# Kernel tuning notes

Hardware: AMD Instinct MI355X
Metric: run time of the kernel (lower is better)

## Reference

```python
import jax, jax.numpy as jnp
import numpy as np
from jax import lax

DN = ('NHWC', 'HWIO', 'NHWC')
NEG = -1e30  # stand-in for -inf at inactive sites during masked max-pool


def setup_inputs() -> dict:
    key = jax.random.key(0)
    ks = jax.random.split(key, 6)
    B, H, W, Cin = 1024, 21, 21, 200
    x = jax.random.normal(ks[0], (B, H, W, Cin), dtype=jnp.float32)
    mask = jax.random.randint(ks[1], (B, H, W), 0, 2, dtype=jnp.int32)
    W1 = jax.random.normal(ks[2], (2, 2, Cin, 16), dtype=jnp.float32) * 0.05
    W2 = jax.random.normal(ks[3], (5, 5, 16, 32), dtype=jnp.float32) * 0.05
    Wlin = jax.random.normal(ks[4], (32, 2), dtype=jnp.float32) * 0.1
    blin = jax.random.normal(ks[5], (2,), dtype=jnp.float32) * 0.1
    return {"x": x, "mask": mask, "W1": W1, "W2": W2, "Wlin": Wlin, "blin": blin}


def _masked_maxpool(h, m, win, stride):
    # scn.MaxPooling: max over ACTIVE sites in window; output site active iff any input active.
    hm = jnp.where(m > 0, h, NEG)
    out = lax.reduce_window(hm, NEG, lax.max, (1, win, win, 1), (1, stride, stride, 1), 'VALID')
    m_out = lax.reduce_window(m, 0.0, lax.max, (1, win, win, 1), (1, stride, stride, 1), 'VALID')
    return jnp.where(m_out > 0, out, 0.0), m_out


def reference(x, mask, W1, W2, Wlin, blin):
    m = mask.astype(x.dtype)[..., None]          # [B,21,21,1] active-site mask
    h = x * m                                    # inactive sites carry zero features
    # SubmanifoldConvolution(2, 200, 16, filter=2): size-preserving, gathers only
    # active neighbors (zeros elsewhere), outputs only at input active sites.
    h = lax.conv_general_dilated(h, W1, (1, 1), [(0, 1), (0, 1)], dimension_numbers=DN)
    h = h * m                                    # [B,21,21,16]
    # MaxPooling(2, 3, 3): 21 -> 7
    h, m = _masked_maxpool(h, m, 3, 3)
    # Convolution(2, 16, 32, filter=5, stride=1): 7 -> 3; output active iff any
    # active input in receptive field; value = sum over active inputs (== dense conv on masked feats).
    h = lax.conv_general_dilated(h, W2, (1, 1), 'VALID', dimension_numbers=DN)
    m = lax.reduce_window(m, 0.0, lax.max, (1, 5, 5, 1), (1, 1, 1, 1), 'VALID')
    h = h * m                                    # [B,3,3,32]
    # MaxPooling(2, 3, 1): 3 -> 1
    h, m = _masked_maxpool(h, m, 3, 1)           # [B,1,1,32]
    # SparseToDense already dense here; view(-1, 32), Linear(32,2), softmax(dim=1)
    h = h.reshape(-1, 32)
    return jax.nn.softmax(h @ Wlin + blin, axis=-1)   # [B,2]
```

## Files before the change

### kernel.cpp

```cpp
#include <hip/hip_runtime.h>
#include <math.h>


#define NEGINF -1e30f

__device__ __forceinline__ int f2o(float f) {
    int i = __float_as_int(f);
    return (i >= 0) ? i : (i ^ 0x7FFFFFFF);
}
__device__ __forceinline__ float o2f(int o) {
    return __int_as_float((o >= 0) ? o : (o ^ 0x7FFFFFFF));
}

__global__ __launch_bounds__(512, 4) void conv1_pool_kernel(
    const float* __restrict__ x,
    const int*   __restrict__ mask,
    const float* __restrict__ W1,
    float* __restrict__ h2,
    float* __restrict__ m2)
{
    __shared__ float w1s[4 * 200 * 16];
    __shared__ unsigned char msk[2 * 441];
    __shared__ unsigned short act[2 * 441];
    __shared__ int h2ord[2][49][16];
    __shared__ int nact;

    const int t  = threadIdx.x;
    const int b0 = blockIdx.x * 2;

    {
        const float4* __restrict__ wg = (const float4*)W1;
        float4* wl = (float4*)w1s;
        for (int v = t; v < 3200; v += 512) wl[v] = wg[v];
    }
    if (t == 0) nact = 0;
    for (int v = t; v < 2 * 49 * 16; v += 512) ((int*)h2ord)[v] = 0x80000000;
    __syncthreads();

    for (int v = t; v < 2 * 441; v += 512) {
        const int b2 = (v >= 441) ? 1 : 0;
        const int p  = v - b2 * 441;
        const int mv = mask[(size_t)(b0 + b2) * 441 + p];
        msk[v] = (unsigned char)(mv != 0);
        if (mv != 0) {
            const int idx = atomicAdd(&nact, 1);
            act[idx] = (unsigned short)v;
        }
    }
    __syncthreads();

    const int na = nact;
    for (int idx = t; idx < na; idx += 512) {
        const int u  = act[idx];
        const int b2 = (u >= 441) ? 1 : 0;
        const int p  = u - b2 * 441;
        const int i  = p / 21;
        const int j  = p - i * 21;
        const float* __restrict__ xb = x + (size_t)(b0 + b2) * 441 * 200;

        float acc[16];
        #pragma unroll
        for (int c = 0; c < 16; ++c) acc[c] = 0.0f;

        #pragma unroll
        for (int tap = 0; tap < 4; ++tap) {
            const int ii = i + (tap >> 1);
            const int jj = j + (tap & 1);
            if (ii < 21 && jj < 21 && msk[b2 * 441 + ii * 21 + jj]) {
                const float4* __restrict__ xp = (const float4*)(xb + (ii * 21 + jj) * 200);
                const float4* wp = ((const float4*)w1s) + tap * 800;

                #pragma unroll 2
                for (int k4 = 0; k4 < 50; ++k4) {
                    const float4 xv = xp[k4];
                    #pragma unroll
                    for (int q = 0; q < 4; ++q) {
                        const float xs = (q == 0) ? xv.x : (q == 1) ? xv.y
                                       : (q == 2) ? xv.z : xv.w;
                        const int kb = (k4 * 4 + q) * 4;
                        const float4 w0 = wp[kb + 0];
                        const float4 w1 = wp[kb + 1];
                        const float4 w2 = wp[kb + 2];
                        const float4 w3 = wp[kb + 3];
                        acc[0]  = fmaf(xs, w0.x, acc[0]);
                        acc[1]  = fmaf(xs, w0.y, acc[1]);
                        acc[2]  = fmaf(xs, w0.z, acc[2]);
                        acc[3]  = fmaf(xs, w0.w, acc[3]);
                        acc[4]  = fmaf(xs, w1.x, acc[4]);
                        acc[5]  = fmaf(xs, w1.y, acc[5]);
                        acc[6]  = fmaf(xs, w1.z, acc[6]);
                        acc[7]  = fmaf(xs, w1.w, acc[7]);
                        acc[8]  = fmaf(xs, w2.x, acc[8]);
                        acc[9]  = fmaf(xs, w2.y, acc[9]);
                        acc[10] = fmaf(xs, w2.z, acc[10]);
                        acc[11] = fmaf(xs, w2.w, acc[11]);
                        acc[12] = fmaf(xs, w3.x, acc[12]);
                        acc[13] = fmaf(xs, w3.y, acc[13]);
                        acc[14] = fmaf(xs, w3.z, acc[14]);
                        acc[15] = fmaf(xs, w3.w, acc[15]);
                    }
                }
            }
        }

        const int cell = (i / 3) * 7 + (j / 3);
        int* dst = &h2ord[b2][cell][0];
        #pragma unroll
        for (int c = 0; c < 16; ++c) atomicMax(&dst[c], f2o(acc[c]));
    }
    __syncthreads();

    for (int v = t; v < 2 * 49 * 16; v += 512) {
        const int b2   = (v >= 784) ? 1 : 0;
        const int r    = v - b2 * 784;
        const int cell = r >> 4;
        const int ch   = r & 15;
        const int pr = cell / 7, pc = cell - pr * 7;
        const unsigned char* mrow = &msk[b2 * 441 + (pr * 3) * 21 + pc * 3];
        int any = 0;
        #pragma unroll
        for (int rr = 0; rr < 3; ++rr)
            any |= mrow[rr * 21 + 0] | mrow[rr * 21 + 1] | mrow[rr * 21 + 2];
        const float val = any ? o2f(h2ord[b2][cell][ch]) : 0.0f;
        h2[(size_t)((b0 + b2) * 49 + cell) * 16 + ch] = val;
        if (ch == 0) m2[(b0 + b2) * 49 + cell] = any ? 1.0f : 0.0f;
    }
}

__global__ __launch_bounds__(256) void tail_kernel(
    const float* __restrict__ h2,
    const float* __restrict__ m2,
    const float* __restrict__ W2,
    const float* __restrict__ Wlin,
    const float* __restrict__ blin,
    float* __restrict__ out)
{
    __shared__ float h2s[49][16];
    __shared__ float m2s[49];
    __shared__ float hc[9][32];
    __shared__ float m3s[9];
    __shared__ float h4[32];

    const int b = blockIdx.x;
    const int t = threadIdx.x;

    for (int t2 = t; t2 < 784; t2 += 256)
        h2s[t2 >> 4][t2 & 15] = h2[(size_t)b * 784 + t2];
    if (t < 49) m2s[t] = m2[b * 49 + t];
    __syncthreads();

    for (int t2 = t; t2 < 288; t2 += 256) {
        const int cell = t2 >> 5;
        const int oc   = t2 & 31;
        const int ci = cell / 3, cj = cell - ci * 3;
        float acc = 0.0f;
        float mm = 0.0f;
        #pragma unroll
        for (int di = 0; di < 5; ++di) {
            #pragma unroll
            for (int dj = 0; dj < 5; ++dj) {
                const int s = (ci + di) * 7 + (cj + dj);
                mm = fmaxf(mm, m2s[s]);
                const float* __restrict__ wrow = W2 + ((di * 5 + dj) * 16) * 32 + oc;
                #pragma unroll
                for (int c = 0; c < 16; ++c)
                    acc = fmaf(h2s[s][c], wrow[c * 32], acc);
            }
        }
        hc[cell][oc] = (mm > 0.0f) ? acc : 0.0f;
        if (oc == 0) m3s[cell] = mm;
    }
    __syncthreads();

    if (t < 32) {
        float best = NEGINF;
        bool any = false;
        #pragma unroll
        for (int cell = 0; cell < 9; ++cell) {
            if (m3s[cell] > 0.0f) {
                any = true;
                best = fmaxf(best, hc[cell][t]);
            }
        }
        h4[t] = any ? best : 0.0f;
    }
    __syncthreads();

    if (t == 0) {
        float l0 = blin[0], l1 = blin[1];
        #pragma unroll
        for (int c = 0; c < 32; ++c) {
            l0 = fmaf(h4[c], Wlin[c * 2 + 0], l0);
            l1 = fmaf(h4[c], Wlin[c * 2 + 1], l1);
        }
        const float mx = fmaxf(l0, l1);
        const float e0 = expf(l0 - mx);
        const float e1 = expf(l1 - mx);
        const float inv = 1.0f / (e0 + e1);
        out[b * 2 + 0] = e0 * inv;
        out[b * 2 + 1] = e1 * inv;
    }
}

extern "C" void kernel_launch(void* const* d_in, const int* in_sizes, int n_in,
                              void* d_out, int out_size, void* d_ws, size_t ws_size,
                              hipStream_t stream) {
    const float* x    = (const float*)d_in[0];
    const int*   mask = (const int*)d_in[1];
    const float* W1   = (const float*)d_in[2];
    const float* W2   = (const float*)d_in[3];
    const float* Wlin = (const float*)d_in[4];
    const float* blin = (const float*)d_in[5];
    float* out = (float*)d_out;

    float* h2 = (float*)d_ws;
    float* m2 = h2 + 1024 * 49 * 16;

    conv1_pool_kernel<<<512, 512, 0, stream>>>(x, mask, W1, h2, m2);
    tail_kernel<<<1024, 256, 0, stream>>>(h2, m2, W2, Wlin, blin, out);
}
```

Measured before the change: 611.7 us.

## Split conv1 into global compacted worklist with two-site register blocking

Adds a compaction kernel that builds a global list of active sites across all batches. The conv1 kernel then processes two active sites per thread in a grid-stride loop, which balances load across blocks and reuses each shared-memory weight read for two sites. The max-pool moves into the tail kernel, which reads a full-resolution h1 buffer. This costs an extra kernel launch, a memset, a global atomic, and an h1 write and read through global memory. It also drops the shared-memory atomicMax pooling.

```diff
diff --git a/kernel.cpp b/kernel.cpp
--- a/kernel.cpp
+++ b/kernel.cpp
@@ -3,138 +3,139 @@
 
 
 #define NEGINF -1e30f
-
-__device__ __forceinline__ int f2o(float f) {
-    int i = __float_as_int(f);
-    return (i >= 0) ? i : (i ^ 0x7FFFFFFF);
-}
-__device__ __forceinline__ float o2f(int o) {
-    return __int_as_float((o >= 0) ? o : (o ^ 0x7FFFFFFF));
-}
-
-__global__ __launch_bounds__(512, 4) void conv1_pool_kernel(
+#define H1_ELEMS (1024 * 441 * 16)
+#define WL_ELEMS (1024 * 441)
+
+__global__ __launch_bounds__(256) void compact_kernel(
+    const int* __restrict__ mask,
+    int* __restrict__ wl,
+    int* __restrict__ nact)
+{
+    __shared__ unsigned short loc[441];
+    __shared__ int cnt, base;
+    const int b = blockIdx.x;
+    const int t = threadIdx.x;
+    if (t == 0) cnt = 0;
+    __syncthreads();
+    for (int p = t; p < 441; p += 256)
+        if (mask[b * 441 + p] != 0) loc[atomicAdd(&cnt, 1)] = (unsigned short)p;
+    __syncthreads();
+    if (t == 0) base = atomicAdd(nact, cnt);
+    __syncthreads();
+    const int n = cnt, bs = base, off = b * 441;
+    for (int k = t; k < n; k += 256) wl[bs + k] = off + loc[k];
+}
+
+__global__ __launch_bounds__(256, 4) void conv1_kernel(
     const float* __restrict__ x,
     const int*   __restrict__ mask,
     const float* __restrict__ W1,
-    float* __restrict__ h2,
-    float* __restrict__ m2)
+    const int*   __restrict__ wl,
+    const int*   __restrict__ nact,
+    float* __restrict__ h1)
 {
     __shared__ float w1s[4 * 200 * 16];
-    __shared__ unsigned char msk[2 * 441];
-    __shared__ unsigned short act[2 * 441];
-    __shared__ int h2ord[2][49][16];
-    __shared__ int nact;
-
-    const int t  = threadIdx.x;
-    const int b0 = blockIdx.x * 2;
 
     {
         const float4* __restrict__ wg = (const float4*)W1;
-        float4* wl = (float4*)w1s;
-        for (int v = t; v < 3200; v += 512) wl[v] = wg[v];
-    }
-    if (t == 0) nact = 0;
-    for (int v = t; v < 2 * 49 * 16; v += 512) ((int*)h2ord)[v] = 0x80000000;
-    __syncthreads();
-
-    for (int v = t; v < 2 * 441; v += 512) {
-        const int b2 = (v >= 441) ? 1 : 0;
-        const int p  = v - b2 * 441;
-        const int mv = mask[(size_t)(b0 + b2) * 441 + p];
-        msk[v] = (unsigned char)(mv != 0);
-        if (mv != 0) {
-            const int idx = atomicAdd(&nact, 1);
-            act[idx] = (unsigned short)v;
-        }
-    }
-    __syncthreads();
-
-    const int na = nact;
-    for (int idx = t; idx < na; idx += 512) {
-        const int u  = act[idx];
-        const int b2 = (u >= 441) ? 1 : 0;
-        const int p  = u - b2 * 441;
-        const int i  = p / 21;
-        const int j  = p - i * 21;
-        const float* __restrict__ xb = x + (size_t)(b0 + b2) * 441 * 200;
-
-        float acc[16];
-        #pragma unroll
-        for (int c = 0; c < 16; ++c) acc[c] = 0.0f;
+        float4* wd = (float4*)w1s;
+        for (int v = threadIdx.x; v < 3200; v += 256) wd[v] = wg[v];
+    }
+    __syncthreads();
+
+    const int n = *nact;
+    const int gtid = blockIdx.x * 256 + threadIdx.x;
+    const int gstride = gridDim.x * 256;
+
+    for (int pair = gtid * 2; pair < n; pair += gstride * 2) {
+        const int iA = wl[pair];
+        const int iB = wl[min(pair + 1, n - 1)];
+
+        const int bA = iA / 441, pA = iA - bA * 441;
+        const int bB = iB / 441, pB = iB - bB * 441;
+        const int ia = pA / 21, ja = pA - ia * 21;
+        const int ib = pB / 21, jb = pB - ib * 21;
+
+        float accA[16], accB[16];
+        #pragma unroll
+        for (int c = 0; c < 16; ++c) { accA[c] = 0.0f; accB[c] = 0.0f; }
 
         #pragma unroll
         for (int tap = 0; tap < 4; ++tap) {
-            const int ii = i + (tap >> 1);
-            const int jj = j + (tap & 1);
-            if (ii < 21 && jj < 21 && msk[b2 * 441 + ii * 21 + jj]) {
-                const float4* __restrict__ xp = (const float4*)(xb + (ii * 21 + jj) * 200);
-                const float4* wp = ((const float4*)w1s) + tap * 800;
-
-                #pragma unroll 2
-                for (int k4 = 0; k4 < 50; ++k4) {
-                    const float4 xv = xp[k4];
-                    #pragma unroll
-                    for (int q = 0; q < 4; ++q) {
-                        const float xs = (q == 0) ? xv.x : (q == 1) ? xv.y
-                                       : (q == 2) ? xv.z : xv.w;
-                        const int kb = (k4 * 4 + q) * 4;
-                        const float4 w0 = wp[kb + 0];
-                        const float4 w1 = wp[kb + 1];
-                        const float4 w2 = wp[kb + 2];
-                        const float4 w3 = wp[kb + 3];
-                        acc[0]  = fmaf(xs, w0.x, acc[0]);
-                        acc[1]  = fmaf(xs, w0.y, acc[1]);
-                        acc[2]  = fmaf(xs, w0.z, acc[2]);
-                        acc[3]  = fmaf(xs, w0.w, acc[3]);
-                        acc[4]  = fmaf(xs, w1.x, acc[4]);
-                        acc[5]  = fmaf(xs, w1.y, acc[5]);
-                        acc[6]  = fmaf(xs, w1.z, acc[6]);
-                        acc[7]  = fmaf(xs, w1.w, acc[7]);
-                        acc[8]  = fmaf(xs, w2.x, acc[8]);
-                        acc[9]  = fmaf(xs, w2.y, acc[9]);
-                        acc[10] = fmaf(xs, w2.z, acc[10]);
-                        acc[11] = fmaf(xs, w2.w, acc[11]);
-                        acc[12] = fmaf(xs, w3.x, acc[12]);
-                        acc[13] = fmaf(xs, w3.y, acc[13]);
-                        acc[14] = fmaf(xs, w3.z, acc[14]);
-                        acc[15] = fmaf(xs, w3.w, acc[15]);
-                    }
+            const int di = tap >> 1, dj = tap & 1;
+
+            const int iiA = ia + di, jjA = ja + dj;
+            const bool vA = (iiA < 21) & (jjA < 21);
+            const int qA = vA ? (iiA * 21 + jjA) : pA;
+            const float mA = (vA && mask[bA * 441 + qA] != 0) ? 1.0f : 0.0f;
+            const float4* __restrict__ pa = (const float4*)(x + (size_t)(bA * 441 + qA) * 200);
+
+            const int iiB = ib + di, jjB = jb + dj;
+            const bool vB = (iiB < 21) & (jjB < 21);
+            const int qB = vB ? (iiB * 21 + jjB) : pB;
+            const float mB = (vB && mask[bB * 441 + qB] != 0) ? 1.0f : 0.0f;
+            const float4* __restrict__ pb = (const float4*)(x + (size_t)(bB * 441 + qB) * 200);
+
+            const float4* wbase = ((const float4*)w1s) + tap * 800;
+
+            #pragma unroll 2
+            for (int k4 = 0; k4 < 50; ++k4) {
+                float4 xa = pa[k4];
+                float4 xb = pb[k4];
+                xa.x *= mA; xa.y *= mA; xa.z *= mA; xa.w *= mA;
+                xb.x *= mB; xb.y *= mB; xb.z *= mB; xb.w *= mB;
+                const float4* wp = wbase + k4 * 16;
+                #pragma unroll
+                for (int q = 0; q < 4; ++q) {
+                    const float xsa = (q == 0) ? xa.x : (q == 1) ? xa.y : (q == 2) ? xa.z : xa.w;
+                    const float xsb = (q == 0) ? xb.x : (q == 1) ? xb.y : (q == 2) ? xb.z : xb.w;
+                    const float4 w0 = wp[q * 4 + 0];
+                    const float4 w1 = wp[q * 4 + 1];
+                    const float4 w2 = wp[q * 4 + 2];
+                    const float4 w3 = wp[q * 4 + 3];
+                    accA[0]  = fmaf(xsa, w0.x, accA[0]);  accB[0]  = fmaf(xsb, w0.x, accB[0]);
+                    accA[1]  = fmaf(xsa, w0.y, accA[1]);  accB[1]  = fmaf(xsb, w0.y, accB[1]);
+                    accA[2]  = fmaf(xsa, w0.z, accA[2]);  accB[2]  = fmaf(xsb, w0.z, accB[2]);
+                    accA[3]  = fmaf(xsa, w0.w, accA[3]);  accB[3]  = fmaf(xsb, w0.w, accB[3]);
+                    accA[4]  = fmaf(xsa, w1.x, accA[4]);  accB[4]  = fmaf(xsb, w1.x, accB[4]);
+                    accA[5]  = fmaf(xsa, w1.y, accA[5]);  accB[5]  = fmaf(xsb, w1.y, accB[5]);
+                    accA[6]  = fmaf(xsa, w1.z, accA[6]);  accB[6]  = fmaf(xsb, w1.z, accB[6]);
+                    accA[7]  = fmaf(xsa, w1.w, accA[7]);  accB[7]  = fmaf(xsb, w1.w, accB[7]);
+                    accA[8]  = fmaf(xsa, w2.x, accA[8]);  accB[8]  = fmaf(xsb, w2.x, accB[8]);
+                    accA[9]  = fmaf(xsa, w2.y, accA[9]);  accB[9]  = fmaf(xsb, w2.y, accB[9]);
+                    accA[10] = fmaf(xsa, w2.z, accA[10]); accB[10] = fmaf(xsb, w2.z, accB[10]);
+                    accA[11] = fmaf(xsa, w2.w, accA[11]); accB[11] = fmaf(xsb, w2.w, accB[11]);
+                    accA[12] = fmaf(xsa, w3.x, accA[12]); accB[12] = fmaf(xsb, w3.x, accB[12]);
+                    accA[13] = fmaf(xsa, w3.y, accA[13]); accB[13] = fmaf(xsb, w3.y, accB[13]);
+                    accA[14] = fmaf(xsa, w3.z, accA[14]); accB[14] = fmaf(xsb, w3.z, accB[14]);
+                    accA[15] = fmaf(xsa, w3.w, accA[15]); accB[15] = fmaf(xsb, w3.w, accB[15]);
                 }
             }
         }
 
-        const int cell = (i / 3) * 7 + (j / 3);
-        int* dst = &h2ord[b2][cell][0];
-        #pragma unroll
-        for (int c = 0; c < 16; ++c) atomicMax(&dst[c], f2o(acc[c]));
-    }
-    __syncthreads();
-
-    for (int v = t; v < 2 * 49 * 16; v += 512) {
-        const int b2   = (v >= 784) ? 1 : 0;
-        const int r    = v - b2 * 784;
-        const int cell = r >> 4;
-        const int ch   = r & 15;
-        const int pr = cell / 7, pc = cell - pr * 7;
-        const unsigned char* mrow = &msk[b2 * 441 + (pr * 3) * 21 + pc * 3];
-        int any = 0;
-        #pragma unroll
-        for (int rr = 0; rr < 3; ++rr)
-            any |= mrow[rr * 21 + 0] | mrow[rr * 21 + 1] | mrow[rr * 21 + 2];
-        const float val = any ? o2f(h2ord[b2][cell][ch]) : 0.0f;
-        h2[(size_t)((b0 + b2) * 49 + cell) * 16 + ch] = val;
-        if (ch == 0) m2[(b0 + b2) * 49 + cell] = any ? 1.0f : 0.0f;
+        float4* dA = (float4*)(h1 + (size_t)iA * 16);
+        dA[0] = make_float4(accA[0],  accA[1],  accA[2],  accA[3]);
+        dA[1] = make_float4(accA[4],  accA[5],  accA[6],  accA[7]);
+        dA[2] = make_float4(accA[8],  accA[9],  accA[10], accA[11]);
+        dA[3] = make_float4(accA[12], accA[13], accA[14], accA[15]);
+        float4* dB = (float4*)(h1 + (size_t)iB * 16);
+        dB[0] = make_float4(accB[0],  accB[1],  accB[2],  accB[3]);
+        dB[1] = make_float4(accB[4],  accB[5],  accB[6],  accB[7]);
+        dB[2] = make_float4(accB[8],  accB[9],  accB[10], accB[11]);
+        dB[3] = make_float4(accB[12], accB[13], accB[14], accB[15]);
     }
 }
 
 __global__ __launch_bounds__(256) void tail_kernel(
-    const float* __restrict__ h2,
-    const float* __restrict__ m2,
+    const float* __restrict__ h1,
+    const int*   __restrict__ mask,
     const float* __restrict__ W2,
     const float* __restrict__ Wlin,
     const float* __restrict__ blin,
     float* __restrict__ out)
 {
+    __shared__ float h1s[441][16];
+    __shared__ unsigned char msk[441];
     __shared__ float h2s[49][16];
     __shared__ float m2s[49];
     __shared__ float hc[9][32];
@@ -144,9 +145,34 @@
     const int b = blockIdx.x;
     const int t = threadIdx.x;
 
-    for (int t2 = t; t2 < 784; t2 += 256)
-        h2s[t2 >> 4][t2 & 15] = h2[(size_t)b * 784 + t2];
-    if (t < 49) m2s[t] = m2[b * 49 + t];
+    for (int p = t; p < 441; p += 256) {
+        const int mv = mask[b * 441 + p];
+        msk[p] = (unsigned char)(mv != 0);
+        if (mv != 0) {
+            const float4* __restrict__ src = (const float4*)(h1 + (size_t)(b * 441 + p) * 16);
+            float4* dst = (float4*)&h1s[p][0];
+            dst[0] = src[0]; dst[1] = src[1]; dst[2] = src[2]; dst[3] = src[3];
+        }
+    }
+    __syncthreads();
+
+    for (int t2 = t; t2 < 784; t2 += 256) {
+        const int cell = t2 >> 4;
+        const int ch   = t2 & 15;
+        const int pr = cell / 7, pc = cell - pr * 7;
+        float best = NEGINF;
+        bool any = false;
+        #pragma unroll
+        for (int r = 0; r < 3; ++r) {
+            #pragma unroll
+            for (int c = 0; c < 3; ++c) {
+                const int s = (pr * 3 + r) * 21 + (pc * 3 + c);
+                if (msk[s]) { any = true; best = fmaxf(best, h1s[s][ch]); }
+            }
+        }
+        h2s[cell][ch] = any ? best : 0.0f;
+        if (ch == 0) m2s[cell] = any ? 1.0f : 0.0f;
+    }
     __syncthreads();
 
     for (int t2 = t; t2 < 288; t2 += 256) {
@@ -177,10 +203,7 @@
         bool any = false;
         #pragma unroll
         for (int cell = 0; cell < 9; ++cell) {
-            if (m3s[cell] > 0.0f) {
-                any = true;
-                best = fmaxf(best, hc[cell][t]);
-            }
+            if (m3s[cell] > 0.0f) { any = true; best = fmaxf(best, hc[cell][t]); }
         }
         h4[t] = any ? best : 0.0f;
     }
@@ -213,9 +236,12 @@
     const float* blin = (const float*)d_in[5];
     float* out = (float*)d_out;
 
-    float* h2 = (float*)d_ws;
-    float* m2 = h2 + 1024 * 49 * 16;
-
-    conv1_pool_kernel<<<512, 512, 0, stream>>>(x, mask, W1, h2, m2);
-    tail_kernel<<<1024, 256, 0, stream>>>(h2, m2, W2, Wlin, blin, out);
-}
+    float* h1   = (float*)d_ws;
+    int*   wl   = (int*)(h1 + H1_ELEMS);
+    int*   nact = wl + WL_ELEMS;
+
+    hipMemsetAsync(nact, 0, sizeof(int), stream);
+    compact_kernel<<<1024, 256, 0, stream>>>(mask, wl, nact);
+    conv1_kernel<<<512, 256, 0, stream>>>(x, mask, W1, wl, nact, h1);
+    tail_kernel<<<1024, 256, 0, stream>>>(h1, mask, W2, Wlin, blin, out);
+}
```

New measurement: 762.5 us. 1.25x slower.
